# Kernel optimization log

Hardware: AMD Instinct MI355X
Metric: run time of the kernel (lower is better)

The kernel has to match this reference:

```python
import jax, jax.numpy as jnp
import numpy as np

N = 8192
H = 512
E = 262144
NUM_LAYERS = 2
LAYER_DECAY = 0.4
INIT_W = 1e-05


def setup_inputs() -> dict:
    key = jax.random.key(0)
    ks = jax.random.split(key, 6)
    x = jax.random.normal(ks[0], (N, H), dtype=jnp.float32)
    rows = jax.random.randint(ks[1], (E,), 0, N, dtype=jnp.int32)
    cols = jax.random.randint(ks[2], (E,), 0, N, dtype=jnp.int32)
    vals = jax.random.uniform(ks[3], (E,), dtype=jnp.float32)
    # near-identity init as in GSS_GNNLayer (torch Linear: y = x @ W.T + b)
    W1 = jax.random.normal(ks[4], (H, H), dtype=jnp.float32) * INIT_W + jnp.eye(H, dtype=jnp.float32)
    b1 = jnp.zeros((H,), dtype=jnp.float32)
    W2 = jax.random.normal(ks[5], (H, H), dtype=jnp.float32) * INIT_W + jnp.eye(H, dtype=jnp.float32)
    b2 = jnp.zeros((H,), dtype=jnp.float32)
    return {"x": x, "rows": rows, "cols": cols, "vals": vals,
            "W1": W1, "b1": b1, "W2": W2, "b2": b2}


def _spmm(rows, cols, vals, dense):
    # sparse [N,N] @ dense [N,H] via gather + segment-sum scatter-add
    return jax.ops.segment_sum(vals[:, None] * dense[cols], rows, num_segments=N)


def _gcn_layer(x, rows, cols, vals, W1, b1, W2, b2):
    Ax = _spmm(rows, cols, vals, x)                      # [N,H]
    pre1 = Ax @ W1.T + b1
    Ax_x = _spmm(rows, cols, vals, Ax * x)               # A(Ax * x)
    pre2 = Ax_x @ W2.T + b2
    pre = pre1 + pre2
    return pre, jax.nn.elu(pre)


def reference(x, rows, cols, vals, W1, b1, W2, b2):
    residual = None
    for _ in range(NUM_LAYERS):  # shared weights across layers, as in source
        pre, x = _gcn_layer(x, rows, cols, vals, W1, b1, W2, b2)
        if residual is not None:
            x = residual + LAYER_DECAY * x
        residual = pre
    # decoder: row-wise L2 normalize (eps=1e-12 like F.normalize), dense gram, relu
    norm = jnp.maximum(jnp.linalg.norm(x, axis=1, keepdims=True), 1e-12)
    hidden_emb = x / norm
    adj_preds = jax.nn.relu(hidden_emb @ hidden_emb.T)   # [N,N]
    return adj_preds, hidden_emb
```

## Files before the change

kernel.cpp:

```cpp
#include <hip/hip_runtime.h>

#define N_NODES 8192
#define HDIM    512
#define NEDGE   262144

typedef __attribute__((ext_vector_type(8))) short bf16x8;
typedef __attribute__((ext_vector_type(4))) float f32x4;

__device__ inline unsigned short f2bf(float f) {
  unsigned u = __float_as_uint(f);
  unsigned r = (u + 0x7FFFu + ((u >> 16) & 1u)) >> 16;
  return (unsigned short)r;
}
__device__ inline float bf2f(short s) {
  return __uint_as_float(((unsigned)(unsigned short)s) << 16);
}

__device__ inline void gload16(const void* g, void* l) {
  __builtin_amdgcn_global_load_lds(
      (const __attribute__((address_space(1))) unsigned*)g,
      (__attribute__((address_space(3))) unsigned*)l, 16, 0, 0);
}

__global__ void zero_kernel(int* __restrict__ p) {
  p[blockIdx.x * 256 + threadIdx.x] = 0;
}

__global__ void hist_kernel(const int* __restrict__ rows, int* __restrict__ counts) {
  int e = blockIdx.x * 256 + threadIdx.x;
  atomicAdd(&counts[rows[e]], 1);
}

__global__ __launch_bounds__(1024) void scan_kernel(const int* __restrict__ counts,
                                                    int* __restrict__ offs,
                                                    int* __restrict__ cursor) {
  __shared__ int s[1024];
  int tid = threadIdx.x;
  int local[8];
  int sum = 0;
#pragma unroll
  for (int i = 0; i < 8; ++i) { local[i] = counts[tid * 8 + i]; sum += local[i]; }
  s[tid] = sum;
  __syncthreads();
  for (int d = 1; d < 1024; d <<= 1) {
    int v = (tid >= d) ? s[tid - d] : 0;
    __syncthreads();
    s[tid] += v;
    __syncthreads();
  }
  int base = (tid > 0) ? s[tid - 1] : 0;
#pragma unroll
  for (int i = 0; i < 8; ++i) {
    offs[tid * 8 + i] = base;
    cursor[tid * 8 + i] = base;
    base += local[i];
  }
  if (tid == 1023) offs[8192] = base;
}

__global__ void scatter_kernel(const int* __restrict__ rows, const int* __restrict__ cols,
                               const float* __restrict__ vals, int* cursor,
                               int2* __restrict__ edges) {
  int e = blockIdx.x * 256 + threadIdx.x;
  int slot = atomicAdd(&cursor[rows[e]], 1);
  edges[slot] = make_int2(cols[e], __float_as_int(vals[e]));
}

template <int MODE>
__global__ __launch_bounds__(256) void spmm_bf(const int* __restrict__ offs,
                                               const int2* __restrict__ edges,
                                               const short* __restrict__ Xbf,
                                               const float* __restrict__ aux,
                                               short* __restrict__ outb,
                                               short* __restrict__ prodb) {
  int row = blockIdx.x * 4 + (threadIdx.x >> 6);
  int lane = threadIdx.x & 63;
  int h0 = lane * 8;
  float acc[8] = {0.f, 0.f, 0.f, 0.f, 0.f, 0.f, 0.f, 0.f};
  int e0 = offs[row], e1 = offs[row + 1];
  int p = e0;
  for (; p + 8 <= e1; p += 8) {
    int2 e[8];
#pragma unroll
    for (int u = 0; u < 8; ++u) e[u] = edges[p + u];
    bf16x8 xv[8];
#pragma unroll
    for (int u = 0; u < 8; ++u)
      xv[u] = *reinterpret_cast<const bf16x8*>(Xbf + (size_t)e[u].x * HDIM + h0);
#pragma unroll
    for (int u = 0; u < 8; ++u) {
      float v = __int_as_float(e[u].y);
#pragma unroll
      for (int j = 0; j < 8; ++j) acc[j] = fmaf(v, bf2f(xv[u][j]), acc[j]);
    }
  }
  for (; p < e1; ++p) {
    int2 e = edges[p];
    float v = __int_as_float(e.y);
    bf16x8 xr = *reinterpret_cast<const bf16x8*>(Xbf + (size_t)e.x * HDIM + h0);
#pragma unroll
    for (int j = 0; j < 8; ++j) acc[j] = fmaf(v, bf2f(xr[j]), acc[j]);
  }
  bf16x8 o;
#pragma unroll
  for (int j = 0; j < 8; ++j) o[j] = (short)f2bf(acc[j]);
  *reinterpret_cast<bf16x8*>(outb + (size_t)row * 1024 + h0) = o;
  if (MODE != 2) {
    const float4* ap = reinterpret_cast<const float4*>(aux + (size_t)row * HDIM + h0);
    float4 a0 = ap[0], a1 = ap[1];
    float xv[8] = {a0.x, a0.y, a0.z, a0.w, a1.x, a1.y, a1.z, a1.w};
    if (MODE == 1) {
#pragma unroll
      for (int j = 0; j < 8; ++j) xv[j] = xv[j] > 0.f ? xv[j] : expm1f(xv[j]);
    }
    bf16x8 t;
#pragma unroll
    for (int j = 0; j < 8; ++j) t[j] = (short)f2bf(acc[j] * xv[j]);
    *reinterpret_cast<bf16x8*>(prodb + (size_t)row * HDIM + h0) = t;
  }
}

__global__ void cast_kernel(const float* __restrict__ src, short* __restrict__ dst,
                            int ld, int coloff) {
  int t = blockIdx.x * 256 + threadIdx.x;
  int row = t >> 6;
  int c0 = (t & 63) * 8;
  const float4* p = reinterpret_cast<const float4*>(src + (size_t)row * HDIM + c0);
  float4 a = p[0], b = p[1];
  bf16x8 o;
  o[0] = (short)f2bf(a.x); o[1] = (short)f2bf(a.y);
  o[2] = (short)f2bf(a.z); o[3] = (short)f2bf(a.w);
  o[4] = (short)f2bf(b.x); o[5] = (short)f2bf(b.y);
  o[6] = (short)f2bf(b.z); o[7] = (short)f2bf(b.w);
  *reinterpret_cast<bf16x8*>(dst + (size_t)row * ld + coloff + c0) = o;
}

__global__ void bias_kernel(const float* __restrict__ b1, const float* __restrict__ b2,
                            float* __restrict__ b12) {
  int j = blockIdx.x * 256 + threadIdx.x;
  if (j < HDIM) b12[j] = b1[j] + b2[j];
}

__global__ __launch_bounds__(256) void rownorm_kernel(const float* __restrict__ X,
                                                      float* __restrict__ outf,
                                                      short* __restrict__ outb) {
  int row = blockIdx.x * 4 + (threadIdx.x >> 6);
  int lane = threadIdx.x & 63;
  int h0 = lane * 8;
  const float4* p = reinterpret_cast<const float4*>(X + (size_t)row * HDIM + h0);
  float4 a = p[0], b = p[1];
  float s = a.x * a.x + a.y * a.y + a.z * a.z + a.w * a.w +
            b.x * b.x + b.y * b.y + b.z * b.z + b.w * b.w;
#pragma unroll
  for (int off = 1; off < 64; off <<= 1) s += __shfl_xor(s, off, 64);
  float inv = 1.f / fmaxf(sqrtf(s), 1e-12f);
  a.x *= inv; a.y *= inv; a.z *= inv; a.w *= inv;
  b.x *= inv; b.y *= inv; b.z *= inv; b.w *= inv;
  float4* q = reinterpret_cast<float4*>(outf + (size_t)row * HDIM + h0);
  q[0] = a; q[1] = b;
  bf16x8 o;
  o[0] = (short)f2bf(a.x); o[1] = (short)f2bf(a.y);
  o[2] = (short)f2bf(a.z); o[3] = (short)f2bf(a.w);
  o[4] = (short)f2bf(b.x); o[5] = (short)f2bf(b.y);
  o[6] = (short)f2bf(b.z); o[7] = (short)f2bf(b.w);
  *reinterpret_cast<bf16x8*>(outb + (size_t)row * HDIM + h0) = o;
}

template <int MODE>
__global__ __launch_bounds__(256) void gemm_lds(const short* __restrict__ A,
                                                const short* __restrict__ B,
                                                int N, int K, int nbn,
                                                const float* __restrict__ bias,
                                                const float* __restrict__ resid,
                                                float* __restrict__ out0,
                                                short* __restrict__ out1bf) {
  __shared__ __align__(16) short la[128 * 64];
  __shared__ __align__(16) short lb[128 * 64];

  int q = gridDim.x >> 3;
  int id = (blockIdx.x & 7) * q + (blockIdx.x >> 3);
  int bn = (id % nbn) * 128;
  int bm = (id / nbn) * 128;

  int lane = threadIdx.x & 63;
  int wave = threadIdx.x >> 6;

  int rsub = lane >> 3;
  int csrc = (lane & 7) ^ rsub;
  size_t ldkB = (size_t)K * 2;
  const char* gA0 = (const char*)A + (size_t)(bm + wave * 32 + rsub) * ldkB + csrc * 16;
  const char* gB0 = (const char*)B + (size_t)(bn + wave * 32 + rsub) * ldkB + csrc * 16;
  char* lA0 = (char*)la + wave * 4096;
  char* lB0 = (char*)lb + wave * 4096;

  f32x4 zero = {0.f, 0.f, 0.f, 0.f};
  f32x4 acc[4][4];
#pragma unroll
  for (int m = 0; m < 4; ++m)
#pragma unroll
    for (int n = 0; n < 4; ++n) acc[m][n] = zero;

  int rlo = lane & 15;
  int khi = lane >> 4;
  int wm = wave >> 1, wn = wave & 1;

  for (int k0 = 0; k0 < K; k0 += 64) {
    __syncthreads();
#pragma unroll
    for (int j = 0; j < 4; ++j) {
      gload16(gA0 + (size_t)j * 8 * ldkB + (size_t)k0 * 2, lA0 + j * 1024);
      gload16(gB0 + (size_t)j * 8 * ldkB + (size_t)k0 * 2, lB0 + j * 1024);
    }
    __syncthreads();
#pragma unroll
    for (int kk = 0; kk < 2; ++kk) {
      bf16x8 av[4], bv[4];
#pragma unroll
      for (int m = 0; m < 4; ++m) {
        int ra = wm * 64 + m * 16 + rlo;
        int pc = (kk * 4 + khi) ^ (ra & 7);
        av[m] = *reinterpret_cast<const bf16x8*>((const char*)la + ra * 128 + pc * 16);
      }
#pragma unroll
      for (int n = 0; n < 4; ++n) {
        int rb = wn * 64 + n * 16 + rlo;
        int pc = (kk * 4 + khi) ^ (rb & 7);
        bv[n] = *reinterpret_cast<const bf16x8*>((const char*)lb + rb * 128 + pc * 16);
      }
#pragma unroll
      for (int m = 0; m < 4; ++m)
#pragma unroll
        for (int n = 0; n < 4; ++n)
          acc[m][n] = __builtin_amdgcn_mfma_f32_16x16x32_bf16(av[m], bv[n], acc[m][n], 0, 0, 0);
    }
  }

  int obm = bm + wm * 64;
  int obn = bn + wn * 64;
  int crow = (lane >> 4) * 4;
  int ccol = lane & 15;
#pragma unroll
  for (int n = 0; n < 4; ++n) {
    int c = obn + n * 16 + ccol;
    float bc = (MODE == 2) ? 0.f : bias[c];
#pragma unroll
    for (int m = 0; m < 4; ++m) {
#pragma unroll
      for (int v = 0; v < 4; ++v) {
        int r = obm + m * 16 + crow + v;
        size_t idx = (size_t)r * N + c;
        float val = acc[m][n][v];
        if (MODE == 0) {
          float pvl = val + bc;
          out0[idx] = pvl;
          float e = pvl > 0.f ? pvl : expm1f(pvl);
          out1bf[idx] = (short)f2bf(e);
        } else if (MODE == 1) {
          float pvl = val + bc;
          out0[idx] = resid[idx] + 0.4f * (pvl > 0.f ? pvl : expm1f(pvl));
        } else {
          out0[idx] = val > 0.f ? val : 0.f;
        }
      }
    }
  }
}

extern "C" void kernel_launch(void* const* d_in, const int* in_sizes, int n_in,
                              void* d_out, int out_size, void* d_ws, size_t ws_size,
                              hipStream_t stream) {
  const float* x  = (const float*)d_in[0];
  const int* rows = (const int*)d_in[1];
  const int* cols = (const int*)d_in[2];
  const float* vals = (const float*)d_in[3];
  const float* W1 = (const float*)d_in[4];
  const float* b1 = (const float*)d_in[5];
  const float* W2 = (const float*)d_in[6];
  const float* b2 = (const float*)d_in[7];

  float* out_adj = (float*)d_out;
  float* out_hid = out_adj + (size_t)N_NODES * N_NODES;

  char* w = (char*)d_ws;
  size_t off = 0;
  auto alloc = [&](size_t bytes) -> void* {
    void* p = w + off;
    off += (bytes + 255) & ~(size_t)255;
    return p;
  };
  int* counts   = (int*)alloc(8192 * sizeof(int));
  int* offs     = (int*)alloc(8193 * sizeof(int));
  int* cursor   = (int*)alloc(8192 * sizeof(int));
  int2* edges   = (int2*)alloc((size_t)NEDGE * sizeof(int2));
  float* b12    = (float*)alloc(HDIM * sizeof(float));
  short* Xbf    = (short*)alloc((size_t)N_NODES * HDIM * sizeof(short));
  short* Tbf    = (short*)alloc((size_t)N_NODES * HDIM * sizeof(short));
  short* Abuf   = (short*)alloc((size_t)N_NODES * 1024 * sizeof(short));
  short* Bbuf   = (short*)alloc((size_t)512 * 1024 * sizeof(short));
  float* pre1   = (float*)alloc((size_t)N_NODES * HDIM * sizeof(float));
  float* Hf     = (float*)alloc((size_t)N_NODES * HDIM * sizeof(float));
  short* Hbuf   = (short*)alloc((size_t)N_NODES * HDIM * sizeof(short));

  zero_kernel<<<32, 256, 0, stream>>>(counts);
  hist_kernel<<<NEDGE / 256, 256, 0, stream>>>(rows, counts);
  scan_kernel<<<1, 1024, 0, stream>>>(counts, offs, cursor);
  scatter_kernel<<<NEDGE / 256, 256, 0, stream>>>(rows, cols, vals, cursor, edges);

  bias_kernel<<<2, 256, 0, stream>>>(b1, b2, b12);
  cast_kernel<<<(512 * 64) / 256, 256, 0, stream>>>(W1, Bbuf, 1024, 0);
  cast_kernel<<<(512 * 64) / 256, 256, 0, stream>>>(W2, Bbuf, 1024, 512);
  cast_kernel<<<2048, 256, 0, stream>>>(x, Xbf, 512, 0);

  spmm_bf<0><<<2048, 256, 0, stream>>>(offs, edges, Xbf, x, Abuf, Tbf);
  spmm_bf<2><<<2048, 256, 0, stream>>>(offs, edges, Tbf, nullptr, Abuf + 512, nullptr);
  gemm_lds<0><<<256, 256, 0, stream>>>(Abuf, Bbuf, 512, 1024, 4, b12, nullptr, pre1, Xbf);

  spmm_bf<1><<<2048, 256, 0, stream>>>(offs, edges, Xbf, pre1, Abuf, Tbf);
  spmm_bf<2><<<2048, 256, 0, stream>>>(offs, edges, Tbf, nullptr, Abuf + 512, nullptr);
  gemm_lds<1><<<256, 256, 0, stream>>>(Abuf, Bbuf, 512, 1024, 4, b12, pre1, Hf, nullptr);

  rownorm_kernel<<<2048, 256, 0, stream>>>(Hf, out_hid, Hbuf);
  gemm_lds<2><<<4096, 256, 0, stream>>>(Hbuf, Hbuf, 8192, 512, 64, nullptr, nullptr, out_adj, nullptr);
}
```

Measured before the change: 361.4 us.

## Software-pipeline SpMM gathers, fuse prep casts, and supertile the gram GEMM

The SpMM inner loop now works in batches of 4 edges and issues the next batch's edge and row loads before accumulating the current batch, so gather latency overlaps the FMAs. The four small cast and bias kernels are merged into one prep_kernel launch to cut launch overhead. The final gram GEMM maps block ids onto 8x8 supertiles of output tiles to improve L2 reuse of Hbuf. The pipelined loop uses more registers and has a smaller batch than the previous 8-wide unroll, which may reduce how many loads are in flight.

```diff
diff --git a/kernel.cpp b/kernel.cpp
--- a/kernel.cpp
+++ b/kernel.cpp
@@ -79,19 +79,45 @@
   float acc[8] = {0.f, 0.f, 0.f, 0.f, 0.f, 0.f, 0.f, 0.f};
   int e0 = offs[row], e1 = offs[row + 1];
   int p = e0;
-  for (; p + 8 <= e1; p += 8) {
-    int2 e[8];
-#pragma unroll
-    for (int u = 0; u < 8; ++u) e[u] = edges[p + u];
-    bf16x8 xv[8];
-#pragma unroll
-    for (int u = 0; u < 8; ++u)
-      xv[u] = *reinterpret_cast<const bf16x8*>(Xbf + (size_t)e[u].x * HDIM + h0);
-#pragma unroll
-    for (int u = 0; u < 8; ++u) {
-      float v = __int_as_float(e[u].y);
-#pragma unroll
-      for (int j = 0; j < 8; ++j) acc[j] = fmaf(v, bf2f(xv[u][j]), acc[j]);
+
+  int2 ma0, ma1, ma2, ma3;
+  bf16x8 xa0, xa1, xa2, xa3;
+
+  if (p + 4 <= e1) {
+    ma0 = edges[p]; ma1 = edges[p + 1]; ma2 = edges[p + 2]; ma3 = edges[p + 3];
+    xa0 = *reinterpret_cast<const bf16x8*>(Xbf + (size_t)ma0.x * HDIM + h0);
+    xa1 = *reinterpret_cast<const bf16x8*>(Xbf + (size_t)ma1.x * HDIM + h0);
+    xa2 = *reinterpret_cast<const bf16x8*>(Xbf + (size_t)ma2.x * HDIM + h0);
+    xa3 = *reinterpret_cast<const bf16x8*>(Xbf + (size_t)ma3.x * HDIM + h0);
+    p += 4;
+    for (; p + 4 <= e1; p += 4) {
+      int2 mb0 = edges[p], mb1 = edges[p + 1], mb2 = edges[p + 2], mb3 = edges[p + 3];
+      bf16x8 xb0 = *reinterpret_cast<const bf16x8*>(Xbf + (size_t)mb0.x * HDIM + h0);
+      bf16x8 xb1 = *reinterpret_cast<const bf16x8*>(Xbf + (size_t)mb1.x * HDIM + h0);
+      bf16x8 xb2 = *reinterpret_cast<const bf16x8*>(Xbf + (size_t)mb2.x * HDIM + h0);
+      bf16x8 xb3 = *reinterpret_cast<const bf16x8*>(Xbf + (size_t)mb3.x * HDIM + h0);
+      float v0 = __int_as_float(ma0.y), v1 = __int_as_float(ma1.y);
+      float v2 = __int_as_float(ma2.y), v3 = __int_as_float(ma3.y);
+#pragma unroll
+      for (int j = 0; j < 8; ++j) {
+        acc[j] = fmaf(v0, bf2f(xa0[j]), acc[j]);
+        acc[j] = fmaf(v1, bf2f(xa1[j]), acc[j]);
+        acc[j] = fmaf(v2, bf2f(xa2[j]), acc[j]);
+        acc[j] = fmaf(v3, bf2f(xa3[j]), acc[j]);
+      }
+      ma0 = mb0; ma1 = mb1; ma2 = mb2; ma3 = mb3;
+      xa0 = xb0; xa1 = xb1; xa2 = xb2; xa3 = xb3;
+    }
+    {
+      float v0 = __int_as_float(ma0.y), v1 = __int_as_float(ma1.y);
+      float v2 = __int_as_float(ma2.y), v3 = __int_as_float(ma3.y);
+#pragma unroll
+      for (int j = 0; j < 8; ++j) {
+        acc[j] = fmaf(v0, bf2f(xa0[j]), acc[j]);
+        acc[j] = fmaf(v1, bf2f(xa1[j]), acc[j]);
+        acc[j] = fmaf(v2, bf2f(xa2[j]), acc[j]);
+        acc[j] = fmaf(v3, bf2f(xa3[j]), acc[j]);
+      }
     }
   }
   for (; p < e1; ++p) {
@@ -101,6 +127,7 @@
 #pragma unroll
     for (int j = 0; j < 8; ++j) acc[j] = fmaf(v, bf2f(xr[j]), acc[j]);
   }
+
   bf16x8 o;
 #pragma unroll
   for (int j = 0; j < 8; ++j) o[j] = (short)f2bf(acc[j]);
@@ -120,25 +147,40 @@
   }
 }
 
-__global__ void cast_kernel(const float* __restrict__ src, short* __restrict__ dst,
-                            int ld, int coloff) {
-  int t = blockIdx.x * 256 + threadIdx.x;
-  int row = t >> 6;
-  int c0 = (t & 63) * 8;
-  const float4* p = reinterpret_cast<const float4*>(src + (size_t)row * HDIM + c0);
+__device__ inline void cast8(const float* src, short* dst) {
+  const float4* p = reinterpret_cast<const float4*>(src);
   float4 a = p[0], b = p[1];
   bf16x8 o;
   o[0] = (short)f2bf(a.x); o[1] = (short)f2bf(a.y);
   o[2] = (short)f2bf(a.z); o[3] = (short)f2bf(a.w);
   o[4] = (short)f2bf(b.x); o[5] = (short)f2bf(b.y);
   o[6] = (short)f2bf(b.z); o[7] = (short)f2bf(b.w);
-  *reinterpret_cast<bf16x8*>(dst + (size_t)row * ld + coloff + c0) = o;
-}
-
-__global__ void bias_kernel(const float* __restrict__ b1, const float* __restrict__ b2,
+  *reinterpret_cast<bf16x8*>(dst) = o;
+}
+
+__global__ void prep_kernel(const float* __restrict__ x,
+                            const float* __restrict__ W1, const float* __restrict__ W2,
+                            const float* __restrict__ b1, const float* __restrict__ b2,
+                            short* __restrict__ Xbf, short* __restrict__ Bbuf,
                             float* __restrict__ b12) {
-  int j = blockIdx.x * 256 + threadIdx.x;
-  if (j < HDIM) b12[j] = b1[j] + b2[j];
+  int b = blockIdx.x;
+  if (b < 2048) {
+    int t = b * 256 + threadIdx.x;
+    int row = t >> 6, c0 = (t & 63) * 8;
+    cast8(x + (size_t)row * 512 + c0, Xbf + (size_t)row * 512 + c0);
+  } else if (b < 2176) {
+    int t = (b - 2048) * 256 + threadIdx.x;
+    int row = t >> 6, c0 = (t & 63) * 8;
+    cast8(W1 + (size_t)row * 512 + c0, Bbuf + (size_t)row * 1024 + c0);
+  } else if (b < 2304) {
+    int t = (b - 2176) * 256 + threadIdx.x;
+    int row = t >> 6, c0 = (t & 63) * 8;
+    cast8(W2 + (size_t)row * 512 + c0, Bbuf + (size_t)row * 1024 + 512 + c0);
+  } else {
+    int j = threadIdx.x;
+    b12[j] = b1[j] + b2[j];
+    b12[j + 256] = b1[j + 256] + b2[j + 256];
+  }
 }
 
 __global__ __launch_bounds__(256) void rownorm_kernel(const float* __restrict__ X,
@@ -179,8 +221,16 @@
 
   int q = gridDim.x >> 3;
   int id = (blockIdx.x & 7) * q + (blockIdx.x >> 3);
-  int bn = (id % nbn) * 128;
-  int bm = (id / nbn) * 128;
+  int bn, bm;
+  if (MODE == 2) {
+    int sid = id >> 6, wid = id & 63;
+    int srow = sid >> 3, scol = sid & 7;
+    bm = (srow * 8 + (wid >> 3)) * 128;
+    bn = (scol * 8 + (wid & 7)) * 128;
+  } else {
+    bn = (id % nbn) * 128;
+    bm = (id / nbn) * 128;
+  }
 
   int lane = threadIdx.x & 63;
   int wave = threadIdx.x >> 6;
@@ -306,10 +356,7 @@
   scan_kernel<<<1, 1024, 0, stream>>>(counts, offs, cursor);
   scatter_kernel<<<NEDGE / 256, 256, 0, stream>>>(rows, cols, vals, cursor, edges);
 
-  bias_kernel<<<2, 256, 0, stream>>>(b1, b2, b12);
-  cast_kernel<<<(512 * 64) / 256, 256, 0, stream>>>(W1, Bbuf, 1024, 0);
-  cast_kernel<<<(512 * 64) / 256, 256, 0, stream>>>(W2, Bbuf, 1024, 512);
-  cast_kernel<<<2048, 256, 0, stream>>>(x, Xbf, 512, 0);
+  prep_kernel<<<2305, 256, 0, stream>>>(x, W1, W2, b1, b2, Xbf, Bbuf, b12);
 
   spmm_bf<0><<<2048, 256, 0, stream>>>(offs, edges, Xbf, x, Abuf, Tbf);
   spmm_bf<2><<<2048, 256, 0, stream>>>(offs, edges, Tbf, nullptr, Abuf + 512, nullptr);
```

New measurement: 328.2 us. -9.2%, faster.
